# Kernel tuning notes

Measured on AMD Instinct MI355X. Metric: run time of the kernel, lower is better.

Reference implementation:

```python
import jax, jax.numpy as jnp
import numpy as np

B, D, H, OUT = 16384, 4096, 7, 7


def setup_inputs() -> dict:
    key = jax.random.key(0)
    k1, k2, k3, k4 = jax.random.split(key, 4)
    features1 = jax.random.normal(k1, (B, D), dtype=jnp.float32)
    features2 = jax.random.normal(k2, (B, D), dtype=jnp.float32)
    W1 = jax.random.normal(k3, (D, H), dtype=jnp.float32) * (1.0 / np.sqrt(D))
    b1 = jnp.zeros((H,), dtype=jnp.float32)
    W2 = jax.random.normal(k4, (H, OUT), dtype=jnp.float32) * (1.0 / np.sqrt(H))
    b2 = jnp.zeros((OUT,), dtype=jnp.float32)
    return {"features1": features1, "features2": features2,
            "W1": W1, "b1": b1, "W2": W2, "b2": b2}


def reference(features1, features2, W1, b1, W2, b2):
    # Gate MLP (Dropout is inference-mode identity): [B, D] -> [B, 7]
    def mlp(x):
        h = jax.nn.relu(x @ W1 + b1)
        return h @ W2 + b2

    # Per-sample scalar logit for each expert: mean over the 7 gate outputs.
    logit1 = mlp(features1).mean(axis=1)  # [B]
    logit2 = mlp(features2).mean(axis=1)  # [B]

    # Per-sample softmax over the 2 experts (vectorized form of the batch loop).
    alpha = jax.nn.softmax(jnp.stack([logit1, logit2], axis=1), axis=1)  # [B, 2]

    # Weighted 2-expert combine: alpha0 * f1 + alpha1 * f2, shape [B, D].
    return alpha[:, 0:1] * features1 + alpha[:, 1:2] * features2
```

## Files before the change

kernel.cpp:

```cpp
#include <hip/hip_runtime.h>
#include <hip/hip_bf16.h>


constexpr int Dk  = 4096;
constexpr int Hk  = 7;
constexpr int NPAIR = Dk / 512;
constexpr int NWE   = Hk * NPAIR * 64;
constexpr int WPK_WORDS = NWE * 4;
constexpr size_t WS_NEEDED = (size_t)WPK_WORDS * 4 + 64;

constexpr int NTH  = 1024;
constexpr int NBLK = 512;
constexpr int ROWS_PER_SET = 4;

__global__ void gating_prep(const float* __restrict__ W1,
                            const float* __restrict__ b1,
                            const float* __restrict__ W2,
                            const float* __restrict__ b2,
                            unsigned int* __restrict__ wsw)
{
    const int t = blockIdx.x * blockDim.x + threadIdx.x;
    if (t < NWE) {
        const int j    = t / (NPAIR * 64);
        const int kk   = (t / 64) % NPAIR;
        const int lane = t & 63;
        const int vi0  = (2 * kk) * 64 + lane;
        unsigned int w[4];
        #pragma unroll
        for (int h = 0; h < 2; ++h) {
            const int vi = vi0 + h * 64;
            #pragma unroll
            for (int p = 0; p < 2; ++p) {
                const int d0 = 4 * vi + 2 * p;
                const unsigned int lo = (unsigned int)__bfloat16_as_ushort(
                    __float2bfloat16(W1[(long long)d0 * Hk + j]));
                const unsigned int hi = (unsigned int)__bfloat16_as_ushort(
                    __float2bfloat16(W1[(long long)(d0 + 1) * Hk + j]));
                w[h * 2 + p] = lo | (hi << 16);
            }
        }
        reinterpret_cast<uint4*>(wsw)[t] = make_uint4(w[0], w[1], w[2], w[3]);
    }
    if (blockIdx.x == 0 && threadIdx.x == 0) {
        float* c = reinterpret_cast<float*>(wsw) + WPK_WORDS;
        #pragma unroll
        for (int j = 0; j < Hk; ++j) {
            c[j] = b1[j];
            float s = 0.f;
            #pragma unroll
            for (int k = 0; k < Hk; ++k) s += W2[j * Hk + k];
            c[Hk + j] = s;
        }
        float sb2 = 0.f;
        #pragma unroll
        for (int k = 0; k < Hk; ++k) sb2 += b2[k];
        c[14] = sb2;
    }
}

__device__ __forceinline__ float bf_lo(unsigned int u) {
    return __uint_as_float(u << 16);
}
__device__ __forceinline__ float bf_hi(unsigned int u) {
    return __uint_as_float(u & 0xFFFF0000u);
}

__global__ __launch_bounds__(NTH, 8)
void gating_wave(const float* __restrict__ f1,
                 const float* __restrict__ f2,
                 const uint4* __restrict__ wpk,
                 const float* __restrict__ gc,
                 float* __restrict__ out,
                 int rows)
{
    __shared__ uint4 wl[NWE];
    __shared__ float red[2][ROWS_PER_SET][2][Hk][4];

    for (int e = threadIdx.x; e < NWE; e += NTH)
        wl[e] = wpk[e];
    __syncthreads();

    const int wid  = threadIdx.x >> 6;
    const int lane = threadIdx.x & 63;
    const int lrow = wid >> 2;
    const int q    = wid & 3;

    float b1r[Hk], sr[Hk];
    #pragma unroll
    for (int j = 0; j < Hk; ++j) { b1r[j] = gc[j]; sr[j] = gc[Hk + j]; }

    const int nrowsets = (rows + ROWS_PER_SET - 1) / ROWS_PER_SET;
    int p = 0;

    for (int rs = blockIdx.x; rs < nrowsets; rs += gridDim.x, p ^= 1) {
        int row = rs * ROWS_PER_SET + lrow;
        if (row >= rows) row = rows - 1;

        const long long base = (long long)row * Dk;
        const float4* __restrict__ f1v = reinterpret_cast<const float4*>(f1 + base);
        const float4* __restrict__ f2v = reinterpret_cast<const float4*>(f2 + base);

        float4 a[4], b[4];
        #pragma unroll
        for (int i = 0; i < 4; ++i) {
            const int vi = (4 * q + i) * 64 + lane;
            a[i] = f1v[vi];
            b[i] = f2v[vi];
        }
        __builtin_amdgcn_sched_barrier(0);

        float acc1[Hk], acc2[Hk];
        #pragma unroll
        for (int j = 0; j < Hk; ++j) { acc1[j] = 0.f; acc2[j] = 0.f; }

        #pragma unroll
        for (int kk2 = 0; kk2 < 2; ++kk2) {
            const int kk = 2 * q + kk2;
            const float4 xa0 = a[2 * kk2],     xb0 = b[2 * kk2];
            const float4 xa1 = a[2 * kk2 + 1], xb1 = b[2 * kk2 + 1];
            #pragma unroll
            for (int j = 0; j < Hk; ++j) {
                const uint4 u = wl[(j * NPAIR + kk) * 64 + lane];
                const float w0 = bf_lo(u.x), w1 = bf_hi(u.x);
                const float w2 = bf_lo(u.y), w3 = bf_hi(u.y);
                const float w4 = bf_lo(u.z), w5 = bf_hi(u.z);
                const float w6 = bf_lo(u.w), w7 = bf_hi(u.w);
                acc1[j] = fmaf(xa0.x, w0, fmaf(xa0.y, w1,
                          fmaf(xa0.z, w2, fmaf(xa0.w, w3, acc1[j]))));
                acc1[j] = fmaf(xa1.x, w4, fmaf(xa1.y, w5,
                          fmaf(xa1.z, w6, fmaf(xa1.w, w7, acc1[j]))));
                acc2[j] = fmaf(xb0.x, w0, fmaf(xb0.y, w1,
                          fmaf(xb0.z, w2, fmaf(xb0.w, w3, acc2[j]))));
                acc2[j] = fmaf(xb1.x, w4, fmaf(xb1.y, w5,
                          fmaf(xb1.z, w6, fmaf(xb1.w, w7, acc2[j]))));
            }
        }

        #pragma unroll
        for (int j = 0; j < Hk; ++j) {
            acc1[j] += __shfl_xor(acc1[j], 32);
            acc2[j] += __shfl_xor(acc2[j], 32);
        }
        float val[Hk];
        #pragma unroll
        for (int j = 0; j < Hk; ++j)
            val[j] = (lane < 32) ? acc1[j] : acc2[j];
        #pragma unroll
        for (int off = 16; off >= 1; off >>= 1) {
            #pragma unroll
            for (int j = 0; j < Hk; ++j)
                val[j] += __shfl_xor(val[j], off);
        }

        if ((lane & 31) == 0) {
            const int e = lane >> 5;
            #pragma unroll
            for (int j = 0; j < Hk; ++j)
                red[p][lrow][e][j][q] = val[j];
        }
        __syncthreads();

        float l1 = 0.f, l2 = 0.f;
        #pragma unroll
        for (int j = 0; j < Hk; ++j) {
            const float4 r1q = *reinterpret_cast<const float4*>(&red[p][lrow][0][j][0]);
            const float4 r2q = *reinterpret_cast<const float4*>(&red[p][lrow][1][j][0]);
            const float h1 = r1q.x + r1q.y + r1q.z + r1q.w + b1r[j];
            const float h2 = r2q.x + r2q.y + r2q.z + r2q.w + b1r[j];
            l1 = fmaf(fmaxf(h1, 0.f), sr[j], l1);
            l2 = fmaf(fmaxf(h2, 0.f), sr[j], l2);
        }
        const float delta = (l2 - l1) * (1.f / 7.f);
        const float a0 = 1.f / (1.f + expf(delta));
        const float a1 = 1.f - a0;

        float4* __restrict__ ov = reinterpret_cast<float4*>(out + base);
        #pragma unroll
        for (int i = 0; i < 4; ++i) {
            const int vi = (4 * q + i) * 64 + lane;
            float4 o;
            o.x = fmaf(a0, a[i].x, a1 * b[i].x);
            o.y = fmaf(a0, a[i].y, a1 * b[i].y);
            o.z = fmaf(a0, a[i].z, a1 * b[i].z);
            o.w = fmaf(a0, a[i].w, a1 * b[i].w);
            ov[vi] = o;
        }
    }
}

__global__ __launch_bounds__(256, 4)
void gating_fused_direct(const float* __restrict__ f1,
                         const float* __restrict__ f2,
                         const float* __restrict__ W1,
                         const float* __restrict__ b1,
                         const float* __restrict__ W2,
                         const float* __restrict__ b2,
                         float* __restrict__ out)
{
    constexpr int VPT = 4;
    const int row = blockIdx.x;
    const int t   = threadIdx.x;
    const long long base = (long long)row * Dk;

    const float4* f1v = reinterpret_cast<const float4*>(f1 + base);
    const float4* f2v = reinterpret_cast<const float4*>(f2 + base);

    float4 r1[VPT], r2[VPT];
    float acc1[Hk], acc2[Hk];
    #pragma unroll
    for (int j = 0; j < Hk; ++j) { acc1[j] = 0.f; acc2[j] = 0.f; }

    #pragma unroll
    for (int k = 0; k < VPT; ++k) {
        const int vi = k * 256 + t;
        r1[k] = f1v[vi];
        r2[k] = f2v[vi];
        const float4* wv = reinterpret_cast<const float4*>(W1 + (long long)vi * 28);
        float4 w4[7];
        #pragma unroll
        for (int q = 0; q < 7; ++q) w4[q] = wv[q];
        const float* ws = reinterpret_cast<const float*>(w4);
        const float* x1 = reinterpret_cast<const float*>(&r1[k]);
        const float* x2 = reinterpret_cast<const float*>(&r2[k]);
        #pragma unroll
        for (int r = 0; r < 4; ++r)
            #pragma unroll
            for (int j = 0; j < Hk; ++j) {
                acc1[j] = fmaf(x1[r], ws[r * 7 + j], acc1[j]);
                acc2[j] = fmaf(x2[r], ws[r * 7 + j], acc2[j]);
            }
    }
    #pragma unroll
    for (int j = 0; j < Hk; ++j)
        #pragma unroll
        for (int off = 32; off >= 1; off >>= 1) {
            acc1[j] += __shfl_down(acc1[j], off);
            acc2[j] += __shfl_down(acc2[j], off);
        }

    __shared__ float red[4][2 * Hk];
    __shared__ float alpha[2];
    const int wave = t >> 6;
    const int lane = t & 63;
    if (lane == 0)
        #pragma unroll
        for (int j = 0; j < Hk; ++j) {
            red[wave][j]      = acc1[j];
            red[wave][Hk + j] = acc2[j];
        }
    __syncthreads();

    if (t == 0) {
        float l1 = 0.f, l2 = 0.f;
        #pragma unroll
        for (int j = 0; j < Hk; ++j) {
            float h1 = red[0][j] + red[1][j] + red[2][j] + red[3][j] + b1[j];
            float h2 = red[0][Hk + j] + red[1][Hk + j] + red[2][Hk + j]
                     + red[3][Hk + j] + b1[j];
            float s = 0.f;
            #pragma unroll
            for (int k2 = 0; k2 < Hk; ++k2) s += W2[j * Hk + k2];
            l1 = fmaf(fmaxf(h1, 0.f), s, l1);
            l2 = fmaf(fmaxf(h2, 0.f), s, l2);
        }
        float sb2 = 0.f;
        #pragma unroll
        for (int k2 = 0; k2 < Hk; ++k2) sb2 += b2[k2];
        l1 = (l1 + sb2) * (1.f / 7.f);
        l2 = (l2 + sb2) * (1.f / 7.f);
        const float a0 = 1.f / (1.f + expf(l2 - l1));
        alpha[0] = a0;
        alpha[1] = 1.f - a0;
    }
    __syncthreads();

    const float a0 = alpha[0];
    const float a1 = alpha[1];
    float4* ov = reinterpret_cast<float4*>(out + base);
    #pragma unroll
    for (int k = 0; k < VPT; ++k) {
        const int vi = k * 256 + t;
        float4 o;
        o.x = a0 * r1[k].x + a1 * r2[k].x;
        o.y = a0 * r1[k].y + a1 * r2[k].y;
        o.z = a0 * r1[k].z + a1 * r2[k].z;
        o.w = a0 * r1[k].w + a1 * r2[k].w;
        ov[vi] = o;
    }
}

extern "C" void kernel_launch(void* const* d_in, const int* in_sizes, int n_in,
                              void* d_out, int out_size, void* d_ws, size_t ws_size,
                              hipStream_t stream) {
    const float* f1 = (const float*)d_in[0];
    const float* f2 = (const float*)d_in[1];
    const float* W1 = (const float*)d_in[2];
    const float* b1 = (const float*)d_in[3];
    const float* W2 = (const float*)d_in[4];
    const float* b2 = (const float*)d_in[5];
    float* out = (float*)d_out;
    const int rows = in_sizes[0] / Dk;

    if (ws_size >= WS_NEEDED) {
        unsigned int* wsw = (unsigned int*)d_ws;
        gating_prep<<<(NWE + 255) / 256, 256, 0, stream>>>(W1, b1, W2, b2, wsw);
        gating_wave<<<NBLK, NTH, 0, stream>>>(
            f1, f2, reinterpret_cast<const uint4*>(wsw),
            reinterpret_cast<const float*>(wsw) + WPK_WORDS, out, rows);
    } else {
        gating_fused_direct<<<rows, 256, 0, stream>>>(f1, f2, W1, b1, W2, b2, out);
    }
}
```

Before: 169.6 us.

## Software-prefetch next row set and use contiguous per-block row chunks

The gating kernel now gives each block a contiguous chunk of row sets instead of a grid-stride loop. It loads the next row set's features into registers while the current one is being reduced and combined, so load latency overlaps compute. Block size drops from 1024 to 512 threads, with two rows per set instead of four, and launch bounds change to match. The prefetch doubles the feature registers held per thread, which may lower occupancy. The new row count assumes rows divide evenly by the set size, and the old tail clamp is gone.

Result: slower. 182.5 us (+7.6%).

```diff
diff --git a/kernel.cpp b/kernel.cpp
--- a/kernel.cpp
+++ b/kernel.cpp
@@ -9,9 +9,9 @@
 constexpr int WPK_WORDS = NWE * 4;
 constexpr size_t WS_NEEDED = (size_t)WPK_WORDS * 4 + 64;
 
-constexpr int NTH  = 1024;
+constexpr int NTH  = 512;
 constexpr int NBLK = 512;
-constexpr int ROWS_PER_SET = 4;
+constexpr int RPS  = 2;
 
 __global__ void gating_prep(const float* __restrict__ W1,
                             const float* __restrict__ b1,
@@ -65,7 +65,7 @@
     return __uint_as_float(u & 0xFFFF0000u);
 }
 
-__global__ __launch_bounds__(NTH, 8)
+__global__ __launch_bounds__(NTH, 2)
 void gating_wave(const float* __restrict__ f1,
                  const float* __restrict__ f2,
                  const uint4* __restrict__ wpk,
@@ -74,7 +74,7 @@
                  int rows)
 {
     __shared__ uint4 wl[NWE];
-    __shared__ float red[2][ROWS_PER_SET][2][Hk][4];
+    __shared__ float red[2][RPS][2][Hk][4];
 
     for (int e = threadIdx.x; e < NWE; e += NTH)
         wl[e] = wpk[e];
@@ -89,23 +89,43 @@
     #pragma unroll
     for (int j = 0; j < Hk; ++j) { b1r[j] = gc[j]; sr[j] = gc[Hk + j]; }
 
-    const int nrowsets = (rows + ROWS_PER_SET - 1) / ROWS_PER_SET;
+    const int nrowsets = rows / RPS;
+    const int chunk    = (nrowsets + NBLK - 1) / NBLK;
+    const int rs_begin = blockIdx.x * chunk;
+    const int rs_end   = min(rs_begin + chunk, nrowsets);
+    const int cnt      = rs_end - rs_begin;
+    if (cnt <= 0) return;
+
+    const int vq0 = 4 * q * 64 + lane;
+
+    float4 a[4], b[4];
+    {
+        const long long base = (long long)(rs_begin * RPS + lrow) * Dk;
+        const float4* f1v = reinterpret_cast<const float4*>(f1 + base);
+        const float4* f2v = reinterpret_cast<const float4*>(f2 + base);
+        #pragma unroll
+        for (int i = 0; i < 4; ++i) {
+            a[i] = f1v[vq0 + i * 64];
+            b[i] = f2v[vq0 + i * 64];
+        }
+    }
+    __builtin_amdgcn_sched_barrier(0);
+
     int p = 0;
-
-    for (int rs = blockIdx.x; rs < nrowsets; rs += gridDim.x, p ^= 1) {
-        int row = rs * ROWS_PER_SET + lrow;
-        if (row >= rows) row = rows - 1;
-
-        const long long base = (long long)row * Dk;
-        const float4* __restrict__ f1v = reinterpret_cast<const float4*>(f1 + base);
-        const float4* __restrict__ f2v = reinterpret_cast<const float4*>(f2 + base);
-
-        float4 a[4], b[4];
-        #pragma unroll
-        for (int i = 0; i < 4; ++i) {
-            const int vi = (4 * q + i) * 64 + lane;
-            a[i] = f1v[vi];
-            b[i] = f2v[vi];
+    for (int it = 0; it < cnt; ++it, p ^= 1) {
+        const int rs = rs_begin + it;
+        const long long base = (long long)(rs * RPS + lrow) * Dk;
+
+        float4 na[4], nb[4];
+        if (it + 1 < cnt) {
+            const long long nbase = (long long)((rs + 1) * RPS + lrow) * Dk;
+            const float4* nf1 = reinterpret_cast<const float4*>(f1 + nbase);
+            const float4* nf2 = reinterpret_cast<const float4*>(f2 + nbase);
+            #pragma unroll
+            for (int i = 0; i < 4; ++i) {
+                na[i] = nf1[vq0 + i * 64];
+                nb[i] = nf2[vq0 + i * 64];
+            }
         }
         __builtin_amdgcn_sched_barrier(0);
 
@@ -177,14 +197,16 @@
         float4* __restrict__ ov = reinterpret_cast<float4*>(out + base);
         #pragma unroll
         for (int i = 0; i < 4; ++i) {
-            const int vi = (4 * q + i) * 64 + lane;
             float4 o;
             o.x = fmaf(a0, a[i].x, a1 * b[i].x);
             o.y = fmaf(a0, a[i].y, a1 * b[i].y);
             o.z = fmaf(a0, a[i].z, a1 * b[i].z);
             o.w = fmaf(a0, a[i].w, a1 * b[i].w);
-            ov[vi] = o;
-        }
+            ov[vq0 + i * 64] = o;
+        }
+
+        #pragma unroll
+        for (int i = 0; i < 4; ++i) { a[i] = na[i]; b[i] = nb[i]; }
     }
 }
 
```

## Replace persistent LDS-weight kernel with one-shot blocks holding weights in registers

Applied to the files above, without the earlier changes.

Drops the persistent grid-stride loop, where 512 blocks each staged the packed bf16 W1 into LDS. Each 512-thread block now handles two rows and loads only its own slice of the packed weights directly into registers from global memory (L2-resident). This removes the per-block LDS staging and the LDS reads in the inner loop, and lets the hardware scheduler spread 8192 blocks. In exchange, every block re-fetches its weight slice from cache, adds register pressure, and pays per-block launch overhead.

Measured after the change: 146.6 us, median of 2. -13.5%, faster.

```diff
diff --git a/kernel.cpp b/kernel.cpp
--- a/kernel.cpp
+++ b/kernel.cpp
@@ -9,9 +9,8 @@
 constexpr int WPK_WORDS = NWE * 4;
 constexpr size_t WS_NEEDED = (size_t)WPK_WORDS * 4 + 64;
 
-constexpr int NTH  = 1024;
-constexpr int NBLK = 512;
-constexpr int ROWS_PER_SET = 4;
+constexpr int NTH = 512;
+constexpr int RPB = 2;
 
 __global__ void gating_prep(const float* __restrict__ W1,
                             const float* __restrict__ b1,
@@ -65,7 +64,7 @@
     return __uint_as_float(u & 0xFFFF0000u);
 }
 
-__global__ __launch_bounds__(NTH, 8)
+__global__ __launch_bounds__(NTH, 2)
 void gating_wave(const float* __restrict__ f1,
                  const float* __restrict__ f2,
                  const uint4* __restrict__ wpk,
@@ -73,118 +72,111 @@
                  float* __restrict__ out,
                  int rows)
 {
-    __shared__ uint4 wl[NWE];
-    __shared__ float red[2][ROWS_PER_SET][2][Hk][4];
-
-    for (int e = threadIdx.x; e < NWE; e += NTH)
-        wl[e] = wpk[e];
-    __syncthreads();
+    __shared__ float red[RPB][2][Hk][4];
 
     const int wid  = threadIdx.x >> 6;
     const int lane = threadIdx.x & 63;
     const int lrow = wid >> 2;
     const int q    = wid & 3;
-
+    const int vq0  = 4 * q * 64 + lane;
+
+    uint4 wr0[Hk], wr1[Hk];
+    #pragma unroll
+    for (int j = 0; j < Hk; ++j) {
+        wr0[j] = wpk[(j * NPAIR + 2 * q)     * 64 + lane];
+        wr1[j] = wpk[(j * NPAIR + 2 * q + 1) * 64 + lane];
+    }
     float b1r[Hk], sr[Hk];
     #pragma unroll
     for (int j = 0; j < Hk; ++j) { b1r[j] = gc[j]; sr[j] = gc[Hk + j]; }
 
-    const int nrowsets = (rows + ROWS_PER_SET - 1) / ROWS_PER_SET;
-    int p = 0;
-
-    for (int rs = blockIdx.x; rs < nrowsets; rs += gridDim.x, p ^= 1) {
-        int row = rs * ROWS_PER_SET + lrow;
-        if (row >= rows) row = rows - 1;
-
-        const long long base = (long long)row * Dk;
-        const float4* __restrict__ f1v = reinterpret_cast<const float4*>(f1 + base);
-        const float4* __restrict__ f2v = reinterpret_cast<const float4*>(f2 + base);
-
-        float4 a[4], b[4];
-        #pragma unroll
-        for (int i = 0; i < 4; ++i) {
-            const int vi = (4 * q + i) * 64 + lane;
-            a[i] = f1v[vi];
-            b[i] = f2v[vi];
-        }
-        __builtin_amdgcn_sched_barrier(0);
-
-        float acc1[Hk], acc2[Hk];
-        #pragma unroll
-        for (int j = 0; j < Hk; ++j) { acc1[j] = 0.f; acc2[j] = 0.f; }
-
-        #pragma unroll
-        for (int kk2 = 0; kk2 < 2; ++kk2) {
-            const int kk = 2 * q + kk2;
-            const float4 xa0 = a[2 * kk2],     xb0 = b[2 * kk2];
-            const float4 xa1 = a[2 * kk2 + 1], xb1 = b[2 * kk2 + 1];
-            #pragma unroll
-            for (int j = 0; j < Hk; ++j) {
-                const uint4 u = wl[(j * NPAIR + kk) * 64 + lane];
-                const float w0 = bf_lo(u.x), w1 = bf_hi(u.x);
-                const float w2 = bf_lo(u.y), w3 = bf_hi(u.y);
-                const float w4 = bf_lo(u.z), w5 = bf_hi(u.z);
-                const float w6 = bf_lo(u.w), w7 = bf_hi(u.w);
-                acc1[j] = fmaf(xa0.x, w0, fmaf(xa0.y, w1,
-                          fmaf(xa0.z, w2, fmaf(xa0.w, w3, acc1[j]))));
-                acc1[j] = fmaf(xa1.x, w4, fmaf(xa1.y, w5,
-                          fmaf(xa1.z, w6, fmaf(xa1.w, w7, acc1[j]))));
-                acc2[j] = fmaf(xb0.x, w0, fmaf(xb0.y, w1,
-                          fmaf(xb0.z, w2, fmaf(xb0.w, w3, acc2[j]))));
-                acc2[j] = fmaf(xb1.x, w4, fmaf(xb1.y, w5,
-                          fmaf(xb1.z, w6, fmaf(xb1.w, w7, acc2[j]))));
-            }
-        }
-
+    int row = blockIdx.x * RPB + lrow;
+    if (row >= rows) row = rows - 1;
+    const long long base = (long long)row * Dk;
+    const float4* __restrict__ f1v = reinterpret_cast<const float4*>(f1 + base);
+    const float4* __restrict__ f2v = reinterpret_cast<const float4*>(f2 + base);
+
+    float4 a[4], b[4];
+    #pragma unroll
+    for (int i = 0; i < 4; ++i) {
+        a[i] = f1v[vq0 + i * 64];
+        b[i] = f2v[vq0 + i * 64];
+    }
+    __builtin_amdgcn_sched_barrier(0);
+
+    float acc1[Hk], acc2[Hk];
+    #pragma unroll
+    for (int j = 0; j < Hk; ++j) { acc1[j] = 0.f; acc2[j] = 0.f; }
+
+    #pragma unroll
+    for (int kk2 = 0; kk2 < 2; ++kk2) {
+        const float4 xa0 = a[2 * kk2],     xb0 = b[2 * kk2];
+        const float4 xa1 = a[2 * kk2 + 1], xb1 = b[2 * kk2 + 1];
         #pragma unroll
         for (int j = 0; j < Hk; ++j) {
-            acc1[j] += __shfl_xor(acc1[j], 32);
-            acc2[j] += __shfl_xor(acc2[j], 32);
-        }
-        float val[Hk];
+            const uint4 u = kk2 ? wr1[j] : wr0[j];
+            const float w0 = bf_lo(u.x), w1 = bf_hi(u.x);
+            const float w2 = bf_lo(u.y), w3 = bf_hi(u.y);
+            const float w4 = bf_lo(u.z), w5 = bf_hi(u.z);
+            const float w6 = bf_lo(u.w), w7 = bf_hi(u.w);
+            acc1[j] = fmaf(xa0.x, w0, fmaf(xa0.y, w1,
+                      fmaf(xa0.z, w2, fmaf(xa0.w, w3, acc1[j]))));
+            acc1[j] = fmaf(xa1.x, w4, fmaf(xa1.y, w5,
+                      fmaf(xa1.z, w6, fmaf(xa1.w, w7, acc1[j]))));
+            acc2[j] = fmaf(xb0.x, w0, fmaf(xb0.y, w1,
+                      fmaf(xb0.z, w2, fmaf(xb0.w, w3, acc2[j]))));
+            acc2[j] = fmaf(xb1.x, w4, fmaf(xb1.y, w5,
+                      fmaf(xb1.z, w6, fmaf(xb1.w, w7, acc2[j]))));
+        }
+    }
+
+    #pragma unroll
+    for (int j = 0; j < Hk; ++j) {
+        acc1[j] += __shfl_xor(acc1[j], 32);
+        acc2[j] += __shfl_xor(acc2[j], 32);
+    }
+    float val[Hk];
+    #pragma unroll
+    for (int j = 0; j < Hk; ++j)
+        val[j] = (lane < 32) ? acc1[j] : acc2[j];
+    #pragma unroll
+    for (int off = 16; off >= 1; off >>= 1) {
         #pragma unroll
         for (int j = 0; j < Hk; ++j)
-            val[j] = (lane < 32) ? acc1[j] : acc2[j];
-        #pragma unroll
-        for (int off = 16; off >= 1; off >>= 1) {
-            #pragma unroll
-            for (int j = 0; j < Hk; ++j)
-                val[j] += __shfl_xor(val[j], off);
-        }
-
-        if ((lane & 31) == 0) {
-            const int e = lane >> 5;
-            #pragma unroll
-            for (int j = 0; j < Hk; ++j)
-                red[p][lrow][e][j][q] = val[j];
-        }
-        __syncthreads();
-
-        float l1 = 0.f, l2 = 0.f;
-        #pragma unroll
-        for (int j = 0; j < Hk; ++j) {
-            const float4 r1q = *reinterpret_cast<const float4*>(&red[p][lrow][0][j][0]);
-            const float4 r2q = *reinterpret_cast<const float4*>(&red[p][lrow][1][j][0]);
-            const float h1 = r1q.x + r1q.y + r1q.z + r1q.w + b1r[j];
-            const float h2 = r2q.x + r2q.y + r2q.z + r2q.w + b1r[j];
-            l1 = fmaf(fmaxf(h1, 0.f), sr[j], l1);
-            l2 = fmaf(fmaxf(h2, 0.f), sr[j], l2);
-        }
-        const float delta = (l2 - l1) * (1.f / 7.f);
-        const float a0 = 1.f / (1.f + expf(delta));
-        const float a1 = 1.f - a0;
-
-        float4* __restrict__ ov = reinterpret_cast<float4*>(out + base);
-        #pragma unroll
-        for (int i = 0; i < 4; ++i) {
-            const int vi = (4 * q + i) * 64 + lane;
-            float4 o;
-            o.x = fmaf(a0, a[i].x, a1 * b[i].x);
-            o.y = fmaf(a0, a[i].y, a1 * b[i].y);
-            o.z = fmaf(a0, a[i].z, a1 * b[i].z);
-            o.w = fmaf(a0, a[i].w, a1 * b[i].w);
-            ov[vi] = o;
-        }
+            val[j] += __shfl_xor(val[j], off);
+    }
+
+    if ((lane & 31) == 0) {
+        const int e = lane >> 5;
+        #pragma unroll
+        for (int j = 0; j < Hk; ++j)
+            red[lrow][e][j][q] = val[j];
+    }
+    __syncthreads();
+
+    float l1 = 0.f, l2 = 0.f;
+    #pragma unroll
+    for (int j = 0; j < Hk; ++j) {
+        const float4 r1q = *reinterpret_cast<const float4*>(&red[lrow][0][j][0]);
+        const float4 r2q = *reinterpret_cast<const float4*>(&red[lrow][1][j][0]);
+        const float h1 = r1q.x + r1q.y + r1q.z + r1q.w + b1r[j];
+        const float h2 = r2q.x + r2q.y + r2q.z + r2q.w + b1r[j];
+        l1 = fmaf(fmaxf(h1, 0.f), sr[j], l1);
+        l2 = fmaf(fmaxf(h2, 0.f), sr[j], l2);
+    }
+    const float delta = (l2 - l1) * (1.f / 7.f);
+    const float a0 = 1.f / (1.f + expf(delta));
+    const float a1 = 1.f - a0;
+
+    float4* __restrict__ ov = reinterpret_cast<float4*>(out + base);
+    #pragma unroll
+    for (int i = 0; i < 4; ++i) {
+        float4 o;
+        o.x = fmaf(a0, a[i].x, a1 * b[i].x);
+        o.y = fmaf(a0, a[i].y, a1 * b[i].y);
+        o.z = fmaf(a0, a[i].z, a1 * b[i].z);
+        o.w = fmaf(a0, a[i].w, a1 * b[i].w);
+        ov[vq0 + i * 64] = o;
     }
 }
 
@@ -218,7 +210,7 @@
         const float4* wv = reinterpret_cast<const float4*>(W1 + (long long)vi * 28);
         float4 w4[7];
         #pragma unroll
-        for (int q = 0; q < 7; ++q) w4[q] = wv[q];
+        for (int qq = 0; qq < 7; ++qq) w4[qq] = wv[qq];
         const float* ws = reinterpret_cast<const float*>(w4);
         const float* x1 = reinterpret_cast<const float*>(&r1[k]);
         const float* x2 = reinterpret_cast<const float*>(&r2[k]);
@@ -304,7 +296,8 @@
     if (ws_size >= WS_NEEDED) {
         unsigned int* wsw = (unsigned int*)d_ws;
         gating_prep<<<(NWE + 255) / 256, 256, 0, stream>>>(W1, b1, W2, b2, wsw);
-        gating_wave<<<NBLK, NTH, 0, stream>>>(
+        const int blocks = (rows + RPB - 1) / RPB;
+        gating_wave<<<blocks, NTH, 0, stream>>>(
             f1, f2, reinterpret_cast<const uint4*>(wsw),
             reinterpret_cast<const float*>(wsw) + WPK_WORDS, out, rows);
     } else {
```
